# Optimization experiments

Measured on AMD Instinct MI355X. Metric: run time of the kernel, lower is better.

## Reference

```python
import jax, jax.numpy as jnp
import numpy as np

NUM_EMBEDDINGS = 1024
EMBEDDING_DIM = 64
COMMITMENT_COST = 0.25


def setup_inputs() -> dict:
    key = jax.random.key(0)
    k1, k2 = jax.random.split(key)
    z = jax.random.normal(k1, (32, EMBEDDING_DIM, 64, 64), dtype=jnp.float32)
    # nn.Embedding weight initialized uniform(-1/K, 1/K)
    lim = 1.0 / NUM_EMBEDDINGS
    codebook = jax.random.uniform(k2, (NUM_EMBEDDINGS, EMBEDDING_DIM),
                                  dtype=jnp.float32, minval=-lim, maxval=lim)
    return {"z": z, "codebook": codebook}


def reference(z, codebook):
    B, D, H, W = z.shape
    # (B, D, H, W) -> (B*H*W, D)
    z_flat = jnp.transpose(z, (0, 2, 3, 1)).reshape(-1, D)
    # squared L2 distances to all codebook entries: (N, K)
    distances = (jnp.sum(z_flat * z_flat, axis=1, keepdims=True)
                 + jnp.sum(codebook * codebook, axis=1)
                 - 2.0 * (z_flat @ codebook.T))
    encoding_indices = jnp.argmin(distances, axis=1)  # (N,)
    z_q = codebook[encoding_indices]                   # (N, D) gather
    z_q = jnp.transpose(z_q.reshape(B, H, W, D), (0, 3, 1, 2))
    vq_loss = jnp.mean((jax.lax.stop_gradient(z_q) - z) ** 2)
    commitment_loss = jnp.mean((z_q - jax.lax.stop_gradient(z)) ** 2)
    loss = vq_loss + COMMITMENT_COST * commitment_loss
    # straight-through estimator
    z_q_st = z + jax.lax.stop_gradient(z_q - z)
    return z_q_st, loss, encoding_indices.reshape(B, H * W)
```

## Files before the change

kernel.cpp:

```cpp
#include <hip/hip_runtime.h>

#define ZN 131072
#define DD 64
#define KK 1024
#define BSTRIDE 262144
#define DSTRIDE 4096
#define ZQ_ELEMS 8388608

#define WS_CSQ_OFF   16
#define WS_ZSQ_OFF   4112
#define WS_CBB_OFF   2363408

#define RF_CAND 16

typedef __attribute__((ext_vector_type(8))) short short8;
typedef __attribute__((ext_vector_type(4))) float f32x4;

__device__ __forceinline__ unsigned short f2bf_rne(float x) {
    unsigned u = __float_as_uint(x);
    return (unsigned short)((u + 0x7fffu + ((u >> 16) & 1u)) >> 16);
}

__device__ __forceinline__ float np_sumsq64(const float* a) {
    float r0 = __fmul_rn(a[0], a[0]), r1 = __fmul_rn(a[1], a[1]);
    float r2 = __fmul_rn(a[2], a[2]), r3 = __fmul_rn(a[3], a[3]);
    float r4 = __fmul_rn(a[4], a[4]), r5 = __fmul_rn(a[5], a[5]);
    float r6 = __fmul_rn(a[6], a[6]), r7 = __fmul_rn(a[7], a[7]);
#pragma unroll
    for (int i = 8; i < 64; i += 8) {
        r0 = __fadd_rn(r0, __fmul_rn(a[i + 0], a[i + 0]));
        r1 = __fadd_rn(r1, __fmul_rn(a[i + 1], a[i + 1]));
        r2 = __fadd_rn(r2, __fmul_rn(a[i + 2], a[i + 2]));
        r3 = __fadd_rn(r3, __fmul_rn(a[i + 3], a[i + 3]));
        r4 = __fadd_rn(r4, __fmul_rn(a[i + 4], a[i + 4]));
        r5 = __fadd_rn(r5, __fmul_rn(a[i + 5], a[i + 5]));
        r6 = __fadd_rn(r6, __fmul_rn(a[i + 6], a[i + 6]));
        r7 = __fadd_rn(r7, __fmul_rn(a[i + 7], a[i + 7]));
    }
    return __fadd_rn(__fadd_rn(__fadd_rn(r0, r1), __fadd_rn(r2, r3)),
                     __fadd_rn(__fadd_rn(r4, r5), __fadd_rn(r6, r7)));
}

__global__ __launch_bounds__(256) void vq_csq(const float* __restrict__ cb,
                                              float* __restrict__ csq) {
    int k = blockIdx.x * 256 + threadIdx.x;
    csq[k] = np_sumsq64(cb + k * DD);
}

__global__ __launch_bounds__(256) void vq_prep_b(const float* __restrict__ cb,
                                                 unsigned short* __restrict__ cbB) {
    int i = blockIdx.x * 256 + threadIdx.x;
    int k = i >> 6, d = i & 63;
    float c = cb[i];
    unsigned short hi = f2bf_rne(c);
    float hf = __uint_as_float((unsigned)hi << 16);
    unsigned short lo = f2bf_rne(c - hf);
    int ct = k >> 4, col = k & 15;
    int s = d >> 5, lg = (d >> 3) & 3, j = d & 7;
    int lane = col + 16 * lg;
    int base = ct * 2048 + s * 512 + lane * 8 + j;
    cbB[base] = hi;
    cbB[base + 1024] = lo;
}

__global__ __launch_bounds__(256) void vq_zsq(const float* __restrict__ z,
                                              float* __restrict__ zsq32) {
    int n = blockIdx.x * 256 + threadIdx.x;
    int b = n >> 12, p = n & 4095;
    const float* zp = z + (size_t)b * BSTRIDE + p;
    float r[8];
#pragma unroll
    for (int j = 0; j < 8; ++j) {
        float v = zp[(size_t)j * DSTRIDE];
        r[j] = __fmul_rn(v, v);
    }
#pragma unroll
    for (int i = 8; i < 64; i += 8)
#pragma unroll
        for (int j = 0; j < 8; ++j) {
            float v = zp[(size_t)(i + j) * DSTRIDE];
            r[j] = __fadd_rn(r[j], __fmul_rn(v, v));
        }
    zsq32[n] = __fadd_rn(__fadd_rn(__fadd_rn(r[0], r[1]), __fadd_rn(r[2], r[3])),
                         __fadd_rn(__fadd_rn(r[4], r[5]), __fadd_rn(r[6], r[7])));
}

#define MFMA_DIST(P, Q, A_H0, A_H1, A_L0, A_L1, B0, B1, B2, B3)               \
    P = __builtin_amdgcn_mfma_f32_16x16x32_bf16(A_H0, B0, P, 0, 0, 0);        \
    Q = __builtin_amdgcn_mfma_f32_16x16x32_bf16(A_H0, B2, Q, 0, 0, 0);        \
    P = __builtin_amdgcn_mfma_f32_16x16x32_bf16(A_H1, B1, P, 0, 0, 0);        \
    Q = __builtin_amdgcn_mfma_f32_16x16x32_bf16(A_H1, B3, Q, 0, 0, 0);        \
    P = __builtin_amdgcn_mfma_f32_16x16x32_bf16(A_L0, B0, P, 0, 0, 0);        \
    Q = __builtin_amdgcn_mfma_f32_16x16x32_bf16(A_L1, B1, Q, 0, 0, 0);

__device__ __forceinline__ unsigned long long ref_pack(const float* zp,
                                                       const float* cp,
                                                       float zsqn, float csqk,
                                                       unsigned k) {
    double a0 = 0.0, a1 = 0.0, a2 = 0.0, a3 = 0.0;
#pragma unroll
    for (int d = 0; d < DD; d += 4) {
        a0 = fma((double)zp[(size_t)(d + 0) * DSTRIDE], (double)cp[d + 0], a0);
        a1 = fma((double)zp[(size_t)(d + 1) * DSTRIDE], (double)cp[d + 1], a1);
        a2 = fma((double)zp[(size_t)(d + 2) * DSTRIDE], (double)cp[d + 2], a2);
        a3 = fma((double)zp[(size_t)(d + 3) * DSTRIDE], (double)cp[d + 3], a3);
    }
    double dot = (a0 + a1) + (a2 + a3);
    float twoC = (float)(2.0 * dot);
    float dist = __fsub_rn(__fadd_rn(zsqn, csqk), twoC);
    unsigned ub = __float_as_uint(dist);
    ub = (ub & 0x80000000u) ? ~ub : (ub | 0x80000000u);
    return ((unsigned long long)ub << 32) | k;
}

__global__ __attribute__((amdgpu_waves_per_eu(4, 4))) __launch_bounds__(256)
void vq_scan(const float* __restrict__ z,
             const unsigned short* __restrict__ cbB,
             const float* __restrict__ cb,
             const float* __restrict__ csq,
             const float* __restrict__ zsq32,
             float* __restrict__ idxf_out) {
    __shared__ __align__(16) unsigned short aFrag[4][2][2][64][8];
    __shared__ float scsq[1024];
    __shared__ float rmin1[64], rmin2[64];
    __shared__ int rbest[64];
    __shared__ float rthr[64];
    __shared__ unsigned rtmask[4];
    __shared__ int candCnt[64];
    __shared__ unsigned short candK[64][RF_CAND];
    __shared__ unsigned long long rpack[64];

    int t = threadIdx.x;
    int n0 = blockIdx.x * 64;
    int b = n0 >> 12, p0 = n0 & 4095;

    for (int i = t; i < 1024; i += 256) scsq[i] = csq[i];
    if (t < 64) {
        candCnt[t] = 0;
        rpack[t] = ~0ull;
    }

    {
        int r = t & 63, gb = t >> 6;
        const float* zp = z + (size_t)b * BSTRIDE + p0 + r;
#pragma unroll
        for (int gg = 0; gg < 2; ++gg) {
            int g = (gb << 1) | gg;
            short8 hi8, lo8;
#pragma unroll
            for (int i2 = 0; i2 < 8; ++i2) {
                float v = zp[(size_t)(8 * g + i2) * DSTRIDE];
                unsigned short h = f2bf_rne(v);
                float hf = __uint_as_float((unsigned)h << 16);
                hi8[i2] = (short)h;
                lo8[i2] = (short)f2bf_rne(v - hf);
            }
            int rt = r >> 4, s = g >> 2, lane = (r & 15) + 16 * (g & 3);
            *(short8*)&aFrag[rt][s][0][lane][0] = hi8;
            *(short8*)&aFrag[rt][s][1][lane][0] = lo8;
        }
    }
    __syncthreads();

    int l = t & 63;
    int colcode = l & 15;
    int w = __builtin_amdgcn_readfirstlane(t >> 6);

    short8 aH0 = *(const short8*)&aFrag[w][0][0][l][0];
    short8 aH1 = *(const short8*)&aFrag[w][1][0][l][0];
    short8 aL0 = *(const short8*)&aFrag[w][0][1][l][0];
    short8 aL1 = *(const short8*)&aFrag[w][1][1][l][0];

    float m1[4], m2[4];
    int bst[4];
#pragma unroll
    for (int r = 0; r < 4; ++r) {
        m1[r] = 3.4e38f;
        m2[r] = 3.4e38f;
        bst[r] = 0;
    }

    const unsigned short* bpb = cbB + (l << 3);
    short8 nb0 = *(const short8*)(bpb);
    short8 nb1 = *(const short8*)(bpb + 512);
    short8 nb2 = *(const short8*)(bpb + 1024);
    short8 nb3 = *(const short8*)(bpb + 1536);
    for (int ph = 0; ph < 8; ++ph) {
        __syncthreads();
#pragma unroll 2
        for (int c8 = 0; c8 < 8; ++c8) {
            int ct = (ph << 3) | c8;
            short8 b0 = nb0, b1 = nb1, b2 = nb2, b3 = nb3;
            if (ct < 63) {
                const unsigned short* np = bpb + (ct + 1) * 2048;
                nb0 = *(const short8*)(np);
                nb1 = *(const short8*)(np + 512);
                nb2 = *(const short8*)(np + 1024);
                nb3 = *(const short8*)(np + 1536);
            }
            float cs = scsq[(ct << 4) + colcode];
            int code = (ct << 4) + colcode;
            f32x4 p = {0.f, 0.f, 0.f, 0.f}, q = {0.f, 0.f, 0.f, 0.f};
            MFMA_DIST(p, q, aH0, aH1, aL0, aL1, b0, b1, b2, b3)
#pragma unroll
            for (int r = 0; r < 4; ++r) {
                float dist = fmaf(-2.f, p[r] + q[r], cs);
                bool lt = dist < m1[r];
                m2[r] = lt ? m1[r] : fminf(m2[r], dist);
                bst[r] = lt ? code : bst[r];
                m1[r] = lt ? dist : m1[r];
            }
        }
    }

#pragma unroll
    for (int m = 1; m <= 8; m <<= 1) {
#pragma unroll
        for (int r = 0; r < 4; ++r) {
            float o1 = __shfl_xor(m1[r], m, 64);
            float o2 = __shfl_xor(m2[r], m, 64);
            int ob = __shfl_xor(bst[r], m, 64);
            bool take = (o1 < m1[r]) || (o1 == m1[r] && ob < bst[r]);
            float n2 = take ? fminf(o2, m1[r]) : fminf(m2[r], o1);
            m1[r] = take ? o1 : m1[r];
            bst[r] = take ? ob : bst[r];
            m2[r] = n2;
        }
    }

#pragma unroll
    for (int r = 0; r < 4; ++r)
        if (colcode == r) {
            int row = (w << 4) + ((l >> 4) << 2) + r;
            rmin1[row] = m1[r];
            rmin2[row] = m2[r];
            rbest[row] = bst[r];
        }
    __syncthreads();

    if (t < 64) {
        bool flag = (rmin2[t] - rmin1[t] < 2e-4f);
        rthr[t] = flag ? rmin1[t] + 2e-4f : -3.4e38f;
        unsigned long long mb = __ballot(flag);
        if (t == 0) {
            rtmask[0] = (unsigned)(mb & 0xFFFFull);
            rtmask[1] = (unsigned)((mb >> 16) & 0xFFFFull);
            rtmask[2] = (unsigned)((mb >> 32) & 0xFFFFull);
            rtmask[3] = (unsigned)((mb >> 48) & 0xFFFFull);
        }
    }
    __syncthreads();

    for (int rt = 0; rt < 4; ++rt) {
        unsigned fm = __builtin_amdgcn_readfirstlane(rtmask[rt]);
        if (fm == 0) continue;
        short8 cH0 = *(const short8*)&aFrag[rt][0][0][l][0];
        short8 cH1 = *(const short8*)&aFrag[rt][1][0][l][0];
        short8 cL0 = *(const short8*)&aFrag[rt][0][1][l][0];
        short8 cL1 = *(const short8*)&aFrag[rt][1][1][l][0];
        int rowb = (rt << 4) + ((l >> 4) << 2);
        float th0 = rthr[rowb + 0], th1 = rthr[rowb + 1];
        float th2 = rthr[rowb + 2], th3 = rthr[rowb + 3];
        for (int ci = 0; ci < 16; ++ci) {
            int ct = (w << 4) + ci;
            const unsigned short* bp = cbB + ct * 2048 + (l << 3);
            short8 b0 = *(const short8*)(bp);
            short8 b1 = *(const short8*)(bp + 512);
            short8 b2 = *(const short8*)(bp + 1024);
            short8 b3 = *(const short8*)(bp + 1536);
            float cs = scsq[(ct << 4) + colcode];
            unsigned code = (unsigned)((ct << 4) + colcode);
            f32x4 p = {0.f, 0.f, 0.f, 0.f}, q = {0.f, 0.f, 0.f, 0.f};
            MFMA_DIST(p, q, cH0, cH1, cL0, cL1, b0, b1, b2, b3)
            float d0 = fmaf(-2.f, p[0] + q[0], cs);
            float d1 = fmaf(-2.f, p[1] + q[1], cs);
            float d2 = fmaf(-2.f, p[2] + q[2], cs);
            float d3 = fmaf(-2.f, p[3] + q[3], cs);
            if (d0 < th0) {
                int pos = atomicAdd(&candCnt[rowb + 0], 1);
                if (pos < RF_CAND) candK[rowb + 0][pos] = (unsigned short)code;
            }
            if (d1 < th1) {
                int pos = atomicAdd(&candCnt[rowb + 1], 1);
                if (pos < RF_CAND) candK[rowb + 1][pos] = (unsigned short)code;
            }
            if (d2 < th2) {
                int pos = atomicAdd(&candCnt[rowb + 2], 1);
                if (pos < RF_CAND) candK[rowb + 2][pos] = (unsigned short)code;
            }
            if (d3 < th3) {
                int pos = atomicAdd(&candCnt[rowb + 3], 1);
                if (pos < RF_CAND) candK[rowb + 3][pos] = (unsigned short)code;
            }
        }
    }
    __syncthreads();

    for (int i = t; i < 64 * RF_CAND; i += 256) {
        int r = i >> 4, sIdx = i & (RF_CAND - 1);
        int cc = candCnt[r];
        if (cc > 0 && cc <= RF_CAND && sIdx < cc) {
            unsigned k = candK[r][sIdx];
            int n = n0 + r;
            const float* zp = z + (size_t)b * BSTRIDE + p0 + r;
            unsigned long long pk = ref_pack(zp, cb + k * DD, zsq32[n], csq[k], k);
            atomicMin(&rpack[r], pk);
        }
    }
    for (int r = 0; r < 64; ++r) {
        if (candCnt[r] > RF_CAND) {
            int n = n0 + r;
            const float* zp = z + (size_t)b * BSTRIDE + p0 + r;
            for (unsigned k = (unsigned)t; k < 1024u; k += 256u) {
                unsigned long long pk = ref_pack(zp, cb + k * DD, zsq32[n], csq[k], k);
                atomicMin(&rpack[r], pk);
            }
        }
    }
    __syncthreads();

    if (t < 64) {
        unsigned long long pk = rpack[t];
        int kk = (pk != ~0ull) ? (int)(unsigned)(pk & 0xFFFFFFFFull) : rbest[t];
        idxf_out[n0 + t] = (float)kk;
    }
}

__global__ __launch_bounds__(256) void vq_gather_loss(const float* __restrict__ z,
                                                      const float* __restrict__ cb,
                                                      const float* __restrict__ idxf,
                                                      float* __restrict__ zq_out,
                                                      double* __restrict__ acc) {
    int n = blockIdx.x * 256 + threadIdx.x;
    int b = n >> 12, p = n & 4095;
    const float* zp = z + (size_t)b * BSTRIDE + p;
    float* qp = zq_out + (size_t)b * BSTRIDE + p;
    int k = (int)idxf[n];
    const float* c = cb + k * DD;

    float s = 0.f;
#pragma unroll
    for (int d = 0; d < DD; ++d) {
        float q = c[d];
        float diff = q - zp[(size_t)d * DSTRIDE];
        s = fmaf(diff, diff, s);
        qp[(size_t)d * DSTRIDE] = q;
    }

#pragma unroll
    for (int off = 32; off; off >>= 1) s += __shfl_down(s, off, 64);
    __shared__ float partial[4];
    if ((threadIdx.x & 63) == 0) partial[threadIdx.x >> 6] = s;
    __syncthreads();
    if (threadIdx.x == 0) {
        float t = (partial[0] + partial[1]) + (partial[2] + partial[3]);
        atomicAdd(acc, (double)t);
    }
}

__global__ void vq_finalize(const double* __restrict__ acc, float* __restrict__ loss_out) {
    *loss_out = (float)(1.25 * (*acc) / (double)ZQ_ELEMS);
}

extern "C" void kernel_launch(void* const* d_in, const int* in_sizes, int n_in,
                              void* d_out, int out_size, void* d_ws, size_t ws_size,
                              hipStream_t stream) {
    const float* z = (const float*)d_in[0];
    const float* cb = (const float*)d_in[1];
    float* out = (float*)d_out;

    float* zq_out = out;
    float* loss_out = out + ZQ_ELEMS;
    float* idxf_out = out + ZQ_ELEMS + 1;

    char* ws = (char*)d_ws;
    double* acc = (double*)ws;
    float* csq = (float*)(ws + WS_CSQ_OFF);
    float* zsq32 = (float*)(ws + WS_ZSQ_OFF);
    unsigned short* cbB = (unsigned short*)(ws + WS_CBB_OFF);

    hipMemsetAsync(d_ws, 0, 16, stream);

    vq_csq<<<KK / 256, 256, 0, stream>>>(cb, csq);
    vq_prep_b<<<KK * DD / 256, 256, 0, stream>>>(cb, cbB);
    vq_zsq<<<ZN / 256, 256, 0, stream>>>(z, zsq32);
    vq_scan<<<ZN / 64, 256, 0, stream>>>(z, cbB, cb, csq, zsq32, idxf_out);
    vq_gather_loss<<<ZN / 256, 256, 0, stream>>>(z, cb, idxf_out, zq_out, acc);
    vq_finalize<<<1, 1, 0, stream>>>(acc, loss_out);
}
```

Measured before the change: 258.4 us.

## Fuse prep, scan, gather-loss and finalize into two kernels with per-lane candidate refinement

Merges the codebook prep kernels into one, drops the separate z-norm pass by recomputing row norms only for ambiguous rows, and fuses the gather/loss and finalize into the scan kernel using a last-block counter. Candidate selection now uses per-lane top-2 mins against a tau threshold via ballots instead of a second MFMA rescan pass. It also removes the software prefetch of the codebook fragments and the waves_per_eu hint. Fewer launches and less redundant z traffic are traded against possibly more exact-refinement work and more register pressure.

```diff
diff --git a/kernel.cpp b/kernel.cpp
--- a/kernel.cpp
+++ b/kernel.cpp
@@ -6,12 +6,10 @@
 #define BSTRIDE 262144
 #define DSTRIDE 4096
 #define ZQ_ELEMS 8388608
+#define TAU 2e-4f
 
 #define WS_CSQ_OFF   16
-#define WS_ZSQ_OFF   4112
 #define WS_CBB_OFF   2363408
-
-#define RF_CAND 16
 
 typedef __attribute__((ext_vector_type(8))) short short8;
 typedef __attribute__((ext_vector_type(4))) float f32x4;
@@ -41,33 +39,7 @@
                      __fadd_rn(__fadd_rn(r4, r5), __fadd_rn(r6, r7)));
 }
 
-__global__ __launch_bounds__(256) void vq_csq(const float* __restrict__ cb,
-                                              float* __restrict__ csq) {
-    int k = blockIdx.x * 256 + threadIdx.x;
-    csq[k] = np_sumsq64(cb + k * DD);
-}
-
-__global__ __launch_bounds__(256) void vq_prep_b(const float* __restrict__ cb,
-                                                 unsigned short* __restrict__ cbB) {
-    int i = blockIdx.x * 256 + threadIdx.x;
-    int k = i >> 6, d = i & 63;
-    float c = cb[i];
-    unsigned short hi = f2bf_rne(c);
-    float hf = __uint_as_float((unsigned)hi << 16);
-    unsigned short lo = f2bf_rne(c - hf);
-    int ct = k >> 4, col = k & 15;
-    int s = d >> 5, lg = (d >> 3) & 3, j = d & 7;
-    int lane = col + 16 * lg;
-    int base = ct * 2048 + s * 512 + lane * 8 + j;
-    cbB[base] = hi;
-    cbB[base + 1024] = lo;
-}
-
-__global__ __launch_bounds__(256) void vq_zsq(const float* __restrict__ z,
-                                              float* __restrict__ zsq32) {
-    int n = blockIdx.x * 256 + threadIdx.x;
-    int b = n >> 12, p = n & 4095;
-    const float* zp = z + (size_t)b * BSTRIDE + p;
+__device__ __forceinline__ float np_sumsq64_strided(const float* zp) {
     float r[8];
 #pragma unroll
     for (int j = 0; j < 8; ++j) {
@@ -81,8 +53,35 @@
             float v = zp[(size_t)(i + j) * DSTRIDE];
             r[j] = __fadd_rn(r[j], __fmul_rn(v, v));
         }
-    zsq32[n] = __fadd_rn(__fadd_rn(__fadd_rn(r[0], r[1]), __fadd_rn(r[2], r[3])),
-                         __fadd_rn(__fadd_rn(r[4], r[5]), __fadd_rn(r[6], r[7])));
+    return __fadd_rn(__fadd_rn(__fadd_rn(r[0], r[1]), __fadd_rn(r[2], r[3])),
+                     __fadd_rn(__fadd_rn(r[4], r[5]), __fadd_rn(r[6], r[7])));
+}
+
+__global__ __launch_bounds__(256) void vq_prep(const float* __restrict__ cb,
+                                               float* __restrict__ csq,
+                                               unsigned short* __restrict__ cbB,
+                                               double* __restrict__ acc,
+                                               unsigned* __restrict__ done) {
+    if (blockIdx.x == 0 && threadIdx.x == 0) {
+        *acc = 0.0;
+        *done = 0u;
+    }
+    int k = blockIdx.x * 256 + threadIdx.x;
+    const float* cp = cb + k * DD;
+    csq[k] = np_sumsq64(cp);
+    int ct = k >> 4, col = k & 15;
+#pragma unroll
+    for (int d = 0; d < DD; ++d) {
+        float c = cp[d];
+        unsigned short hi = f2bf_rne(c);
+        float hf = __uint_as_float((unsigned)hi << 16);
+        unsigned short lo = f2bf_rne(c - hf);
+        int s = d >> 5, lg = (d >> 3) & 3, j = d & 7;
+        int lane = col + 16 * lg;
+        int base = ct * 2048 + s * 512 + lane * 8 + j;
+        cbB[base] = hi;
+        cbB[base + 1024] = lo;
+    }
 }
 
 #define MFMA_DIST(P, Q, A_H0, A_H1, A_L0, A_L1, B0, B1, B2, B3)               \
@@ -113,32 +112,34 @@
     return ((unsigned long long)ub << 32) | k;
 }
 
-__global__ __attribute__((amdgpu_waves_per_eu(4, 4))) __launch_bounds__(256)
-void vq_scan(const float* __restrict__ z,
-             const unsigned short* __restrict__ cbB,
-             const float* __restrict__ cb,
-             const float* __restrict__ csq,
-             const float* __restrict__ zsq32,
-             float* __restrict__ idxf_out) {
+__global__ __launch_bounds__(256)
+void vq_fused(const float* __restrict__ z,
+              const unsigned short* __restrict__ cbB,
+              const float* __restrict__ cb,
+              const float* __restrict__ csq,
+              float* __restrict__ idxf_out,
+              float* __restrict__ zq_out,
+              float* __restrict__ loss_out,
+              double* __restrict__ acc,
+              unsigned* __restrict__ done) {
     __shared__ __align__(16) unsigned short aFrag[4][2][2][64][8];
     __shared__ float scsq[1024];
-    __shared__ float rmin1[64], rmin2[64];
-    __shared__ int rbest[64];
-    __shared__ float rthr[64];
-    __shared__ unsigned rtmask[4];
     __shared__ int candCnt[64];
-    __shared__ unsigned short candK[64][RF_CAND];
+    __shared__ unsigned short candK[64][16];
+    __shared__ unsigned char ovfF[64];
+    __shared__ int ridx[64];
     __shared__ unsigned long long rpack[64];
+    __shared__ int workRows[64];
+    __shared__ int nWork;
+    __shared__ float partial[4];
 
     int t = threadIdx.x;
     int n0 = blockIdx.x * 64;
     int b = n0 >> 12, p0 = n0 & 4095;
 
     for (int i = t; i < 1024; i += 256) scsq[i] = csq[i];
-    if (t < 64) {
-        candCnt[t] = 0;
-        rpack[t] = ~0ull;
-    }
+    if (t == 0) nWork = 0;
+    if (t < 64) rpack[t] = ~0ull;
 
     {
         int r = t & 63, gb = t >> 6;
@@ -180,24 +181,16 @@
         bst[r] = 0;
     }
 
-    const unsigned short* bpb = cbB + (l << 3);
-    short8 nb0 = *(const short8*)(bpb);
-    short8 nb1 = *(const short8*)(bpb + 512);
-    short8 nb2 = *(const short8*)(bpb + 1024);
-    short8 nb3 = *(const short8*)(bpb + 1536);
     for (int ph = 0; ph < 8; ++ph) {
         __syncthreads();
 #pragma unroll 2
         for (int c8 = 0; c8 < 8; ++c8) {
             int ct = (ph << 3) | c8;
-            short8 b0 = nb0, b1 = nb1, b2 = nb2, b3 = nb3;
-            if (ct < 63) {
-                const unsigned short* np = bpb + (ct + 1) * 2048;
-                nb0 = *(const short8*)(np);
-                nb1 = *(const short8*)(np + 512);
-                nb2 = *(const short8*)(np + 1024);
-                nb3 = *(const short8*)(np + 1536);
-            }
+            const unsigned short* bp = cbB + ct * 2048 + (l << 3);
+            short8 b0 = *(const short8*)(bp);
+            short8 b1 = *(const short8*)(bp + 512);
+            short8 b2 = *(const short8*)(bp + 1024);
+            short8 b3 = *(const short8*)(bp + 1536);
             float cs = scsq[(ct << 4) + colcode];
             int code = (ct << 4) + colcode;
             f32x4 p = {0.f, 0.f, 0.f, 0.f}, q = {0.f, 0.f, 0.f, 0.f};
@@ -213,153 +206,108 @@
         }
     }
 
-#pragma unroll
-    for (int m = 1; m <= 8; m <<= 1) {
-#pragma unroll
-        for (int r = 0; r < 4; ++r) {
-            float o1 = __shfl_xor(m1[r], m, 64);
-            float o2 = __shfl_xor(m2[r], m, 64);
-            int ob = __shfl_xor(bst[r], m, 64);
-            bool take = (o1 < m1[r]) || (o1 == m1[r] && ob < bst[r]);
-            float n2 = take ? fminf(o2, m1[r]) : fminf(m2[r], o1);
-            m1[r] = take ? o1 : m1[r];
-            bst[r] = take ? ob : bst[r];
-            m2[r] = n2;
-        }
-    }
-
-#pragma unroll
-    for (int r = 0; r < 4; ++r)
-        if (colcode == r) {
-            int row = (w << 4) + ((l >> 4) << 2) + r;
-            rmin1[row] = m1[r];
-            rmin2[row] = m2[r];
-            rbest[row] = bst[r];
-        }
+    int g = l >> 4;
+#pragma unroll
+    for (int r = 0; r < 4; ++r) {
+        float v = m1[r];
+        v = fminf(v, __shfl_xor(v, 1, 64));
+        v = fminf(v, __shfl_xor(v, 2, 64));
+        v = fminf(v, __shfl_xor(v, 4, 64));
+        v = fminf(v, __shfl_xor(v, 8, 64));
+        float thr = v + TAU;
+        bool mine = (m1[r] < thr);
+        unsigned long long bal1 = __ballot(mine);
+        unsigned long long bal2 = __ballot(m2[r] < thr);
+        unsigned slice1 = (unsigned)((bal1 >> (16 * g)) & 0xFFFFull);
+        unsigned slice2 = (unsigned)((bal2 >> (16 * g)) & 0xFFFFull);
+        int row = (w << 4) + (g << 2) + r;
+        if (mine) {
+            int pos = __popc(slice1 & ((1u << colcode) - 1u));
+            candK[row][pos] = (unsigned short)bst[r];
+        }
+        if (colcode == 0) {
+            candCnt[row] = __popc(slice1);
+            ovfF[row] = (slice2 != 0u) ? 1 : 0;
+        }
+    }
     __syncthreads();
 
     if (t < 64) {
-        bool flag = (rmin2[t] - rmin1[t] < 2e-4f);
-        rthr[t] = flag ? rmin1[t] + 2e-4f : -3.4e38f;
-        unsigned long long mb = __ballot(flag);
-        if (t == 0) {
-            rtmask[0] = (unsigned)(mb & 0xFFFFull);
-            rtmask[1] = (unsigned)((mb >> 16) & 0xFFFFull);
-            rtmask[2] = (unsigned)((mb >> 32) & 0xFFFFull);
-            rtmask[3] = (unsigned)((mb >> 48) & 0xFFFFull);
-        }
-    }
-    __syncthreads();
-
-    for (int rt = 0; rt < 4; ++rt) {
-        unsigned fm = __builtin_amdgcn_readfirstlane(rtmask[rt]);
-        if (fm == 0) continue;
-        short8 cH0 = *(const short8*)&aFrag[rt][0][0][l][0];
-        short8 cH1 = *(const short8*)&aFrag[rt][1][0][l][0];
-        short8 cL0 = *(const short8*)&aFrag[rt][0][1][l][0];
-        short8 cL1 = *(const short8*)&aFrag[rt][1][1][l][0];
-        int rowb = (rt << 4) + ((l >> 4) << 2);
-        float th0 = rthr[rowb + 0], th1 = rthr[rowb + 1];
-        float th2 = rthr[rowb + 2], th3 = rthr[rowb + 3];
-        for (int ci = 0; ci < 16; ++ci) {
-            int ct = (w << 4) + ci;
-            const unsigned short* bp = cbB + ct * 2048 + (l << 3);
-            short8 b0 = *(const short8*)(bp);
-            short8 b1 = *(const short8*)(bp + 512);
-            short8 b2 = *(const short8*)(bp + 1024);
-            short8 b3 = *(const short8*)(bp + 1536);
-            float cs = scsq[(ct << 4) + colcode];
-            unsigned code = (unsigned)((ct << 4) + colcode);
-            f32x4 p = {0.f, 0.f, 0.f, 0.f}, q = {0.f, 0.f, 0.f, 0.f};
-            MFMA_DIST(p, q, cH0, cH1, cL0, cL1, b0, b1, b2, b3)
-            float d0 = fmaf(-2.f, p[0] + q[0], cs);
-            float d1 = fmaf(-2.f, p[1] + q[1], cs);
-            float d2 = fmaf(-2.f, p[2] + q[2], cs);
-            float d3 = fmaf(-2.f, p[3] + q[3], cs);
-            if (d0 < th0) {
-                int pos = atomicAdd(&candCnt[rowb + 0], 1);
-                if (pos < RF_CAND) candK[rowb + 0][pos] = (unsigned short)code;
+        int cnt = candCnt[t];
+        if (cnt == 1 && !ovfF[t]) {
+            ridx[t] = candK[t][0];
+        } else {
+            int wi = atomicAdd(&nWork, 1);
+            workRows[wi] = t;
+        }
+    }
+    __syncthreads();
+
+    int nw = nWork;
+    for (int wi0 = 0; wi0 < nw; wi0 += 16) {
+        int wi = wi0 + (t >> 4);
+        if (wi < nw) {
+            int row = workRows[wi];
+            int c = t & 15;
+            if (!ovfF[row] && c < candCnt[row]) {
+                unsigned k = candK[row][c];
+                const float* zp = z + (size_t)b * BSTRIDE + p0 + row;
+                float zsqn = np_sumsq64_strided(zp);
+                unsigned long long pk =
+                    ref_pack(zp, cb + k * DD, zsqn, scsq[k], k);
+                atomicMin(&rpack[row], pk);
             }
-            if (d1 < th1) {
-                int pos = atomicAdd(&candCnt[rowb + 1], 1);
-                if (pos < RF_CAND) candK[rowb + 1][pos] = (unsigned short)code;
+        }
+    }
+    for (int wi = 0; wi < nw; ++wi) {
+        int row = workRows[wi];
+        if (ovfF[row]) {
+            const float* zp = z + (size_t)b * BSTRIDE + p0 + row;
+            float zsqn = np_sumsq64_strided(zp);
+            for (unsigned k = (unsigned)t; k < 1024u; k += 256u) {
+                unsigned long long pk =
+                    ref_pack(zp, cb + k * DD, zsqn, scsq[k], k);
+                atomicMin(&rpack[row], pk);
             }
-            if (d2 < th2) {
-                int pos = atomicAdd(&candCnt[rowb + 2], 1);
-                if (pos < RF_CAND) candK[rowb + 2][pos] = (unsigned short)code;
-            }
-            if (d3 < th3) {
-                int pos = atomicAdd(&candCnt[rowb + 3], 1);
-                if (pos < RF_CAND) candK[rowb + 3][pos] = (unsigned short)code;
-            }
-        }
-    }
-    __syncthreads();
-
-    for (int i = t; i < 64 * RF_CAND; i += 256) {
-        int r = i >> 4, sIdx = i & (RF_CAND - 1);
-        int cc = candCnt[r];
-        if (cc > 0 && cc <= RF_CAND && sIdx < cc) {
-            unsigned k = candK[r][sIdx];
-            int n = n0 + r;
-            const float* zp = z + (size_t)b * BSTRIDE + p0 + r;
-            unsigned long long pk = ref_pack(zp, cb + k * DD, zsq32[n], csq[k], k);
-            atomicMin(&rpack[r], pk);
-        }
-    }
-    for (int r = 0; r < 64; ++r) {
-        if (candCnt[r] > RF_CAND) {
-            int n = n0 + r;
-            const float* zp = z + (size_t)b * BSTRIDE + p0 + r;
-            for (unsigned k = (unsigned)t; k < 1024u; k += 256u) {
-                unsigned long long pk = ref_pack(zp, cb + k * DD, zsq32[n], csq[k], k);
-                atomicMin(&rpack[r], pk);
-            }
-        }
-    }
-    __syncthreads();
-
+        }
+    }
+    __syncthreads();
     if (t < 64) {
-        unsigned long long pk = rpack[t];
-        int kk = (pk != ~0ull) ? (int)(unsigned)(pk & 0xFFFFFFFFull) : rbest[t];
-        idxf_out[n0 + t] = (float)kk;
-    }
-}
-
-__global__ __launch_bounds__(256) void vq_gather_loss(const float* __restrict__ z,
-                                                      const float* __restrict__ cb,
-                                                      const float* __restrict__ idxf,
-                                                      float* __restrict__ zq_out,
-                                                      double* __restrict__ acc) {
-    int n = blockIdx.x * 256 + threadIdx.x;
-    int b = n >> 12, p = n & 4095;
-    const float* zp = z + (size_t)b * BSTRIDE + p;
-    float* qp = zq_out + (size_t)b * BSTRIDE + p;
-    int k = (int)idxf[n];
-    const float* c = cb + k * DD;
-
-    float s = 0.f;
-#pragma unroll
-    for (int d = 0; d < DD; ++d) {
-        float q = c[d];
-        float diff = q - zp[(size_t)d * DSTRIDE];
-        s = fmaf(diff, diff, s);
-        qp[(size_t)d * DSTRIDE] = q;
-    }
-
-#pragma unroll
-    for (int off = 32; off; off >>= 1) s += __shfl_down(s, off, 64);
-    __shared__ float partial[4];
-    if ((threadIdx.x & 63) == 0) partial[threadIdx.x >> 6] = s;
-    __syncthreads();
-    if (threadIdx.x == 0) {
-        float t = (partial[0] + partial[1]) + (partial[2] + partial[3]);
-        atomicAdd(acc, (double)t);
-    }
-}
-
-__global__ void vq_finalize(const double* __restrict__ acc, float* __restrict__ loss_out) {
-    *loss_out = (float)(1.25 * (*acc) / (double)ZQ_ELEMS);
+        if (rpack[t] != ~0ull) ridx[t] = (int)(unsigned)(rpack[t] & 1023ull);
+        idxf_out[n0 + t] = (float)ridx[t];
+    }
+    __syncthreads();
+
+    {
+        int r = t & 63, dg = t >> 6;
+        int kk = ridx[r];
+        const float* zp = z + (size_t)b * BSTRIDE + p0 + r;
+        float* qp = zq_out + (size_t)b * BSTRIDE + p0 + r;
+        const float* cp = cb + kk * DD;
+        float s = 0.f;
+#pragma unroll
+        for (int dd = dg * 16; dd < dg * 16 + 16; ++dd) {
+            float qv = cp[dd];
+            float diff = qv - zp[(size_t)dd * DSTRIDE];
+            s = fmaf(diff, diff, s);
+            qp[(size_t)dd * DSTRIDE] = qv;
+        }
+#pragma unroll
+        for (int off = 32; off; off >>= 1) s += __shfl_down(s, off, 64);
+        if (l == 0) partial[t >> 6] = s;
+    }
+    __syncthreads();
+    if (t == 0) {
+        float tt = (partial[0] + partial[1]) + (partial[2] + partial[3]);
+        atomicAdd(acc, (double)tt);
+        __threadfence();
+        unsigned v = atomicAdd(done, 1u);
+        if (v == gridDim.x - 1) {
+            __threadfence();
+            double s2 = atomicAdd(acc, 0.0);
+            *loss_out = (float)(1.25 * s2 / (double)ZQ_ELEMS);
+        }
+    }
 }
 
 extern "C" void kernel_launch(void* const* d_in, const int* in_sizes, int n_in,
@@ -375,16 +323,11 @@
 
     char* ws = (char*)d_ws;
     double* acc = (double*)ws;
+    unsigned* done = (unsigned*)(ws + 8);
     float* csq = (float*)(ws + WS_CSQ_OFF);
-    float* zsq32 = (float*)(ws + WS_ZSQ_OFF);
     unsigned short* cbB = (unsigned short*)(ws + WS_CBB_OFF);
 
-    hipMemsetAsync(d_ws, 0, 16, stream);
-
-    vq_csq<<<KK / 256, 256, 0, stream>>>(cb, csq);
-    vq_prep_b<<<KK * DD / 256, 256, 0, stream>>>(cb, cbB);
-    vq_zsq<<<ZN / 256, 256, 0, stream>>>(z, zsq32);
-    vq_scan<<<ZN / 64, 256, 0, stream>>>(z, cbB, cb, csq, zsq32, idxf_out);
-    vq_gather_loss<<<ZN / 256, 256, 0, stream>>>(z, cb, idxf_out, zq_out, acc);
-    vq_finalize<<<1, 1, 0, stream>>>(acc, loss_out);
-}
+    vq_prep<<<KK / 256, 256, 0, stream>>>(cb, csq, cbB, acc, done);
+    vq_fused<<<ZN / 64, 256, 0, stream>>>(z, cbB, cb, csq, idxf_out,
+                                          zq_out, loss_out, acc, done);
+}
```

Result: slower. 346.6 us (+34.1%).
